# Performance work log

Hardware: AMD Instinct MI355X
Metric: run time of the kernel (lower is better)

Reference implementation:

```python
import jax, jax.numpy as jnp
import numpy as np

EPS = 1e-5


def setup_inputs() -> dict:
    key = jax.random.key(0)
    ks = jax.random.split(key, 12)
    B, S, M, D, H, dh = 8, 512, 512, 1024, 16, 64
    T = S + M
    w_scale = 0.03  # keep attention logits in a sane range (mimics nn.Linear init scale)
    return {
        "x": jax.random.normal(ks[0], (B, S, D), jnp.float32),
        "mem": jax.random.normal(ks[1], (B, M, D), jnp.float32),
        "R": jax.random.normal(ks[2], (T, D), jnp.float32),
        "u": jax.random.normal(ks[3], (1, H, 1, dh), jnp.float32) * 0.1,
        "t": jax.random.normal(ks[4], (1, H, 1, dh), jnp.float32) * 0.1,
        "Wq": jax.random.normal(ks[5], (H * dh, D), jnp.float32) * w_scale,
        "Wk": jax.random.normal(ks[6], (H * dh, D), jnp.float32) * w_scale,
        "Wv": jax.random.normal(ks[7], (H * dh, D), jnp.float32) * w_scale,
        "Wr": jax.random.normal(ks[8], (H * dh, D), jnp.float32) * w_scale,
        "Wo": jax.random.normal(ks[9], (D, H * dh), jnp.float32) * w_scale,
        "gamma": jnp.ones((D,), jnp.float32),
        "beta": jnp.zeros((D,), jnp.float32),
    }


def reference(x, mem, R, u, t, Wq, Wk, Wv, Wr, Wo, gamma, beta):
    B, S, D = x.shape
    H, dh = u.shape[1], u.shape[3]
    h = jnp.concatenate([mem, x], axis=1)          # [B, T, D]
    T = h.shape[1]
    M = T - S

    q = (x @ Wq.T).reshape(B, S, H, dh).transpose(0, 2, 1, 3)   # [B,H,S,dh]
    k = (h @ Wk.T).reshape(B, T, H, dh).transpose(0, 2, 1, 3)   # [B,H,T,dh]
    v = (h @ Wv.T).reshape(B, T, H, dh).transpose(0, 2, 1, 3)   # [B,H,T,dh]
    r = (R[-T:] @ Wr.T).reshape(1, T, H, dh).transpose(0, 2, 1, 3)  # [1,H,T,dh]

    ac = jnp.einsum("bhid,bhjd->bhij", q + u, k)                # [B,H,S,T]
    bd = jnp.einsum("bhid,hjd->bhij", q + t, r[0])              # [B,H,S,T]

    # circulant shift: shifted[..., i, j] = bd[..., i, (j - i + S - 1) % T]
    idx = (jnp.arange(T)[None, :] - jnp.arange(S)[:, None] + S - 1) % T  # [S,T]
    bd = jnp.take_along_axis(bd, idx[None, None], axis=3)

    # causal mask with memory offset: keep j <= i + M (tril(mem_len)), then
    # exact-zero entries (the masked ones) become -inf, matching the original.
    mask = jnp.arange(T)[None, :] <= (jnp.arange(S)[:, None] + M)        # [S,T]
    score = jnp.where(mask[None, None], (ac + bd) / jnp.sqrt(jnp.float32(dh)), 0.0)
    score = jnp.where(score == 0, -jnp.inf, score)
    p = jax.nn.softmax(score, axis=-1)                                   # [B,H,S,T]

    att = jnp.einsum("bhij,bhjd->bhid", p, v).transpose(0, 2, 1, 3).reshape(B, S, H * dh)
    out = att @ Wo.T                                                      # dropout is identity (p=0/eval)

    y = out + x
    mu = jnp.mean(y, axis=-1, keepdims=True)
    var = jnp.var(y, axis=-1, keepdims=True)
    return (y - mu) / jnp.sqrt(var + EPS) * gamma + beta
```

## Files before the change

### kernel.cpp

```cpp
#include <hip/hip_runtime.h>
#include <math.h>

#define BB 8
#define SS 512
#define MM 512
#define TT 1024
#define DD 1024
#define HH 16
#define DH 64

typedef __attribute__((ext_vector_type(8))) short bf16x8;
typedef __attribute__((ext_vector_type(4))) float f32x4;

#define SCL2E 0.1803368801111f
#define DTHR 11.5f

__device__ __forceinline__ ushort f2bf(float f) {
  union { float f; unsigned u; } x; x.f = f;
  unsigned r = x.u + 0x7fffu + ((x.u >> 16) & 1u);
  return (ushort)(r >> 16);
}
__device__ __forceinline__ float bf2f(ushort u) {
  return __builtin_bit_cast(float, ((unsigned)u) << 16);
}

__device__ __forceinline__ void stage16(void* lds, const void* g) {
  __builtin_amdgcn_global_load_lds((const __attribute__((address_space(1))) void*)g,
                                   (__attribute__((address_space(3))) void*)lds, 16, 0, 0);
}

template <int C>
__device__ __forceinline__ float dppf(float x) {
  return __builtin_bit_cast(float,
      __builtin_amdgcn_update_dpp(0, __builtin_bit_cast(int, x), C, 0xF, 0xF, true));
}
__device__ __forceinline__ float redmax16(float x) {
  x = fmaxf(x, dppf<0xB1>(x));
  x = fmaxf(x, dppf<0x4E>(x));
  x = fmaxf(x, dppf<0x141>(x));
  x = fmaxf(x, dppf<0x140>(x));
  return x;
}
__device__ __forceinline__ float redsum16(float x) {
  x += dppf<0xB1>(x);
  x += dppf<0x4E>(x);
  x += dppf<0x141>(x);
  x += dppf<0x140>(x);
  return x;
}
__device__ __forceinline__ float bperm_f(int byteaddr, float v) {
  return __builtin_bit_cast(float,
      __builtin_amdgcn_ds_bpermute(byteaddr, __builtin_bit_cast(int, v)));
}

__global__ __launch_bounds__(256) void cast_all(
    const float* __restrict__ mem, const float* __restrict__ x,
    const float* __restrict__ R, const float* __restrict__ Wq,
    const float* __restrict__ Wk, const float* __restrict__ Wv,
    const float* __restrict__ Wr, const float* __restrict__ Wo,
    ushort* __restrict__ hb, ushort* __restrict__ Rb, ushort* __restrict__ Wqb,
    ushort* __restrict__ Wkb, ushort* __restrict__ Wvb, ushort* __restrict__ Wrb,
    ushort* __restrict__ Wob) {
  const int M1 = 1 << 20;
  int i = (blockIdx.x * 256 + threadIdx.x) * 8;
  const float* src;
  ushort* dst;
  if (i < 4 * M1) {
    src = mem + i;
    dst = hb + (size_t)i + (size_t)(i >> 19) * 524288;
  } else if (i < 8 * M1) {
    int j = i - 4 * M1;
    src = x + j;
    dst = hb + (size_t)j + (size_t)(j >> 19) * 524288 + 524288;
  } else if (i < 9 * M1) {
    src = R + (i - 8 * M1);  dst = Rb + (i - 8 * M1);
  } else if (i < 10 * M1) {
    src = Wq + (i - 9 * M1); dst = Wqb + (i - 9 * M1);
  } else if (i < 11 * M1) {
    src = Wk + (i - 10 * M1); dst = Wkb + (i - 10 * M1);
  } else if (i < 12 * M1) {
    src = Wv + (i - 11 * M1); dst = Wvb + (i - 11 * M1);
  } else if (i < 13 * M1) {
    src = Wr + (i - 12 * M1); dst = Wrb + (i - 12 * M1);
  } else {
    src = Wo + (i - 13 * M1); dst = Wob + (i - 13 * M1);
  }
  float4 a = *(const float4*)(src);
  float4 c = *(const float4*)(src + 4);
  union { bf16x8 v; ushort u[8]; } pk;
  pk.u[0] = f2bf(a.x); pk.u[1] = f2bf(a.y); pk.u[2] = f2bf(a.z); pk.u[3] = f2bf(a.w);
  pk.u[4] = f2bf(c.x); pk.u[5] = f2bf(c.y); pk.u[6] = f2bf(c.z); pk.u[7] = f2bf(c.w);
  *(bf16x8*)(void*)dst = pk.v;
}

__global__ __launch_bounds__(256) void gemm_qkvr(
    const ushort* __restrict__ hb, const ushort* __restrict__ Rbuf,
    const ushort* __restrict__ Wqb, const ushort* __restrict__ Wkb,
    const ushort* __restrict__ Wvb, const ushort* __restrict__ Wrb,
    ushort* __restrict__ qub, ushort* __restrict__ qtb,
    ushort* __restrict__ kbo, ushort* __restrict__ vtb, ushort* __restrict__ rbo,
    const float* __restrict__ uvec, const float* __restrict__ tvec) {
  __shared__ ushort As[128 * 32];
  __shared__ ushort Bs[128 * 32];
  const int bid = (blockIdx.x & 7) * 168 + (blockIdx.x >> 3);
  const ushort* A;
  const ushort* W;
  ushort* C0 = nullptr;
  ushort* C1 = nullptr;
  bool dual = false, qslice = false, vmode = false;
  int mt, nx;
  if (bid < 256) {
    int r = bid; mt = r >> 3; nx = r & 7;
    A = hb; W = Wqb; C0 = qub; C1 = qtb; dual = true; qslice = true;
  } else if (bid < 768) {
    int r = bid - 256; mt = r >> 3; nx = r & 7;
    A = hb; W = Wkb; C0 = kbo;
  } else if (bid < 1280) {
    int r = bid - 768; mt = r >> 3; nx = r & 7;
    A = hb; W = Wvb; C0 = vtb; vmode = true;
  } else {
    int r = bid - 1280; mt = r >> 3; nx = r & 7;
    A = Rbuf; W = Wrb; C0 = rbo;
  }
  const int m0 = mt * 128, n0 = nx * 128;

  const int t = threadIdx.x;
  const int w = t >> 6, l = t & 63;
  const int m16 = l & 15, kg = l >> 4;
  const int wr = w >> 1, wc = w & 1;

  const int c0 = t, c1 = t + 256;
  const ushort* asrc0;
  const ushort* asrc1;
  {
    int gm0 = m0 + (c0 >> 2), gm1 = m0 + (c1 >> 2);
    if (qslice) {
      asrc0 = A + ((size_t)((gm0 >> 9) * TT + MM + (gm0 & 511))) * DD + (c0 & 3) * 8;
      asrc1 = A + ((size_t)((gm1 >> 9) * TT + MM + (gm1 & 511))) * DD + (c1 & 3) * 8;
    } else {
      asrc0 = A + (size_t)gm0 * DD + (c0 & 3) * 8;
      asrc1 = A + (size_t)gm1 * DD + (c1 & 3) * 8;
    }
  }
  const ushort* bsrc0 = W + (size_t)(n0 + (c0 >> 2)) * DD + (c0 & 3) * 8;
  const ushort* bsrc1 = W + (size_t)(n0 + (c1 >> 2)) * DD + (c1 & 3) * 8;
  ushort* adst0 = As + c0 * 8;
  ushort* adst1 = As + c1 * 8;
  ushort* bdst0 = Bs + c0 * 8;
  ushort* bdst1 = Bs + c1 * 8;

  f32x4 acc[4][4];
#pragma unroll
  for (int mi = 0; mi < 4; ++mi)
#pragma unroll
    for (int ni = 0; ni < 4; ++ni) acc[mi][ni] = (f32x4){0.f, 0.f, 0.f, 0.f};

  for (int k0 = 0; k0 < DD; k0 += 32) {
    stage16(adst0, asrc0 + k0);
    stage16(adst1, asrc1 + k0);
    stage16(bdst0, bsrc0 + k0);
    stage16(bdst1, bsrc1 + k0);
    __syncthreads();
    bf16x8 af[4], bfr[4];
#pragma unroll
    for (int mi = 0; mi < 4; ++mi)
      af[mi] = *(const bf16x8*)(const void*)&As[(wr * 64 + mi * 16 + m16) * 32 + kg * 8];
#pragma unroll
    for (int ni = 0; ni < 4; ++ni)
      bfr[ni] = *(const bf16x8*)(const void*)&Bs[(wc * 64 + ni * 16 + m16) * 32 + kg * 8];
#pragma unroll
    for (int mi = 0; mi < 4; ++mi)
#pragma unroll
      for (int ni = 0; ni < 4; ++ni)
        acc[mi][ni] = __builtin_amdgcn_mfma_f32_16x16x32_bf16(af[mi], bfr[ni], acc[mi][ni], 0, 0, 0);
    __syncthreads();
  }

  const int rbase = m0 + wr * 64 + kg * 4;
  const int cbase = n0 + wc * 64 + m16;
  if (vmode) {
    const int bb = m0 >> 10;
    const int tt0 = (m0 & 1023) + wr * 64 + kg * 4;
#pragma unroll
    for (int mi = 0; mi < 4; ++mi)
#pragma unroll
      for (int ni = 0; ni < 4; ++ni) {
        ushort4 o;
        o.x = f2bf(acc[mi][ni][0]); o.y = f2bf(acc[mi][ni][1]);
        o.z = f2bf(acc[mi][ni][2]); o.w = f2bf(acc[mi][ni][3]);
        *(ushort4*)(C0 + ((size_t)(bb * 1024 + cbase + ni * 16) << 10) + tt0 + mi * 16) = o;
      }
  } else if (dual) {
    float uv[4], tv[4];
#pragma unroll
    for (int ni = 0; ni < 4; ++ni) { uv[ni] = uvec[cbase + ni * 16]; tv[ni] = tvec[cbase + ni * 16]; }
#pragma unroll
    for (int mi = 0; mi < 4; ++mi)
#pragma unroll
      for (int ni = 0; ni < 4; ++ni)
#pragma unroll
        for (int rg = 0; rg < 4; ++rg) {
          size_t idx = (size_t)(rbase + mi * 16 + rg) * DD + cbase + ni * 16;
          C0[idx] = f2bf(acc[mi][ni][rg] + uv[ni]);
          C1[idx] = f2bf(acc[mi][ni][rg] + tv[ni]);
        }
  } else {
#pragma unroll
    for (int mi = 0; mi < 4; ++mi)
#pragma unroll
      for (int ni = 0; ni < 4; ++ni)
#pragma unroll
        for (int rg = 0; rg < 4; ++rg)
          C0[(size_t)(rbase + mi * 16 + rg) * DD + cbase + ni * 16] = f2bf(acc[mi][ni][rg]);
  }
}

__global__ __launch_bounds__(256) void gemm_wo(const ushort* __restrict__ A,
                                               const ushort* __restrict__ W,
                                               ushort* __restrict__ Cb) {
  __shared__ ushort As[128 * 32];
  __shared__ ushort Bs[128 * 32];
  const int bid = (blockIdx.x & 7) * 32 + (blockIdx.x >> 3);
  const int mt = bid >> 3, nx = bid & 7;
  const int m0 = mt * 128, n0 = nx * 128;
  const int t = threadIdx.x;
  const int w = t >> 6, l = t & 63;
  const int m16 = l & 15, kg = l >> 4;
  const int wr = w >> 1, wc = w & 1;

  const int c0 = t, c1 = t + 256;
  const ushort* asrc0 = A + (size_t)(m0 + (c0 >> 2)) * DD + (c0 & 3) * 8;
  const ushort* asrc1 = A + (size_t)(m0 + (c1 >> 2)) * DD + (c1 & 3) * 8;
  const ushort* bsrc0 = W + (size_t)(n0 + (c0 >> 2)) * DD + (c0 & 3) * 8;
  const ushort* bsrc1 = W + (size_t)(n0 + (c1 >> 2)) * DD + (c1 & 3) * 8;
  ushort* adst0 = As + c0 * 8;
  ushort* adst1 = As + c1 * 8;
  ushort* bdst0 = Bs + c0 * 8;
  ushort* bdst1 = Bs + c1 * 8;

  f32x4 acc[4][4];
#pragma unroll
  for (int mi = 0; mi < 4; ++mi)
#pragma unroll
    for (int ni = 0; ni < 4; ++ni) acc[mi][ni] = (f32x4){0.f, 0.f, 0.f, 0.f};

  for (int k0 = 0; k0 < DD; k0 += 32) {
    stage16(adst0, asrc0 + k0);
    stage16(adst1, asrc1 + k0);
    stage16(bdst0, bsrc0 + k0);
    stage16(bdst1, bsrc1 + k0);
    __syncthreads();
    bf16x8 af[4], bfr[4];
#pragma unroll
    for (int mi = 0; mi < 4; ++mi)
      af[mi] = *(const bf16x8*)(const void*)&As[(wr * 64 + mi * 16 + m16) * 32 + kg * 8];
#pragma unroll
    for (int ni = 0; ni < 4; ++ni)
      bfr[ni] = *(const bf16x8*)(const void*)&Bs[(wc * 64 + ni * 16 + m16) * 32 + kg * 8];
#pragma unroll
    for (int mi = 0; mi < 4; ++mi)
#pragma unroll
      for (int ni = 0; ni < 4; ++ni)
        acc[mi][ni] = __builtin_amdgcn_mfma_f32_16x16x32_bf16(af[mi], bfr[ni], acc[mi][ni], 0, 0, 0);
    __syncthreads();
  }

  const int rbase = m0 + wr * 64 + kg * 4;
  const int cbase = n0 + wc * 64 + m16;
#pragma unroll
  for (int mi = 0; mi < 4; ++mi)
#pragma unroll
    for (int ni = 0; ni < 4; ++ni)
#pragma unroll
      for (int rg = 0; rg < 4; ++rg)
        Cb[(size_t)(rbase + mi * 16 + rg) * DD + cbase + ni * 16] = f2bf(acc[mi][ni][rg]);
}

__global__ __launch_bounds__(256) void attn_mfma(const ushort* __restrict__ qu,
                                                 const ushort* __restrict__ qt,
                                                 const ushort* __restrict__ kb,
                                                 const ushort* __restrict__ vt,
                                                 const ushort* __restrict__ rb,
                                                 ushort* __restrict__ att) {
  const int w = threadIdx.x >> 6;
  const int l = threadIdx.x & 63;
  const int m16 = l & 15;
  const int kg = l >> 4;
  const int bid = blockIdx.x;
  const int it = 7 - (bid >> 7);
  const int bh = bid & 127;
  const int b = bh >> 4, h = bh & 15;
  const int i0 = it * 64;

  __shared__ ushort Ks[2][4096];
  __shared__ ushort Vs[4096];
  __shared__ ushort Rl[8192];
  __shared__ ushort plds[4][16][72];

  bf16x8 aqu[2], aqt[2];
  {
    const ushort* qrow = qu + ((size_t)(b * SS + i0 + w * 16 + m16)) * DD + h * DH + kg * 8;
    aqu[0] = *(const bf16x8*)(const void*)(qrow);
    aqu[1] = *(const bf16x8*)(const void*)(qrow + 32);
    const ushort* qrow2 = qt + ((size_t)(b * SS + i0 + w * 16 + m16)) * DD + h * DH + kg * 8;
    aqt[0] = *(const bf16x8*)(const void*)(qrow2);
    aqt[1] = *(const bf16x8*)(const void*)(qrow2 + 32);
  }

  int baddr[4];
  bool bsel[4];
#pragma unroll
  for (int rg = 0; rg < 4; ++rg) {
    const int rw = kg * 4 + rg;
    baddr[rg] = (kg * 16 + ((m16 + 15 - rw) & 15)) << 2;
    bsel[rg] = m16 > rw;
  }

  const int c0 = threadIdx.x, c1 = threadIdx.x + 256;
  const int r0 = c0 >> 3, sc0 = ((c0 & 7) * 8) ^ ((r0 & 7) << 3);
  const int r1 = c1 >> 3, sc1 = ((c1 & 7) * 8) ^ ((r1 & 7) << 3);
  const ushort* kp0 = kb + ((size_t)(b * TT) + r0) * DD + h * DH + sc0;
  const ushort* kp1 = kb + ((size_t)(b * TT) + r1) * DD + h * DH + sc1;
  const ushort* vp0 = vt + ((size_t)(b * 1024 + h * DH + r0)) * 1024 + sc0;
  const ushort* vp1 = vt + ((size_t)(b * 1024 + h * DH + r1)) * 1024 + sc1;

  const int cb0 = (kg * 8) ^ ((m16 & 7) << 3);
  const int cb1 = (kg * 8 + 32) ^ ((m16 & 7) << 3);
  int slot64[5];
#pragma unroll
  for (int f = 0; f < 5; ++f)
    slot64[f] = ((496 - i0 - w * 16 + m16 + f * 16) & 127) << 6;

  {
    const int base0 = 448 - i0;
#pragma unroll
    for (int kk = 0; kk < 4; ++kk) {
      int c = threadIdx.x + kk * 256;
      int ro = c >> 3, cc = c & 7;
      int p = base0 + ro;
      int slot = p & 127;
      stage16(Rl + slot * 64 + cc * 8,
              rb + (size_t)p * DD + h * DH + ((cc * 8) ^ ((ro & 7) << 3)));
    }
  }
  stage16(&Ks[0][c0 * 8], kp0);
  stage16(&Ks[0][c1 * 8], kp1);
  stage16(Vs + c0 * 8, vp0);
  stage16(Vs + c1 * 8, vp1);
  kp0 += (size_t)64 * DD; kp1 += (size_t)64 * DD;
  vp0 += 64; vp1 += 64;

  f32x4 O[4];
  float mrow[4], lrow[4];
#pragma unroll
  for (int nt = 0; nt < 4; ++nt) O[nt] = (f32x4){0.f, 0.f, 0.f, 0.f};
#pragma unroll
  for (int rg = 0; rg < 4; ++rg) { mrow[rg] = -1e30f; lrow[rg] = 0.f; }

  const int ntj = it + 9;
  int cur = 0;
  for (int jt = 0; jt < ntj; ++jt) {
    const int j0 = jt * 64;

    if (jt > 0) {
      stage16(Vs + c0 * 8, vp0);
      stage16(Vs + c1 * 8, vp1);
      vp0 += 64; vp1 += 64;
      const int pstart = 512 + j0 - i0;
#pragma unroll
      for (int kk = 0; kk < 2; ++kk) {
        int c = threadIdx.x + kk * 256;
        int ro = c >> 3, cc = c & 7;
        int p = pstart + ro;
        int pc = p < 1023 ? p : 1023;
        int slot = p & 127;
        stage16(Rl + slot * 64 + cc * 8,
                rb + (size_t)pc * DD + h * DH + ((cc * 8) ^ ((ro & 7) << 3)));
      }
    }
    __syncthreads();

    const ushort* kbase = &Ks[cur][0];
    f32x4 ac[4];
#pragma unroll
    for (int nt = 0; nt < 4; ++nt) {
      ac[nt] = (f32x4){0.f, 0.f, 0.f, 0.f};
      const int row = nt * 16 + m16;
#pragma unroll
      for (int ks = 0; ks < 2; ++ks) {
        bf16x8 bk = *(const bf16x8*)(const void*)(kbase + row * 64 + (ks == 0 ? cb0 : cb1));
        ac[nt] = __builtin_amdgcn_mfma_f32_16x16x32_bf16(aqu[ks], bk, ac[nt], 0, 0, 0);
      }
    }

    if (jt + 1 < ntj) {
      stage16(&Ks[cur ^ 1][c0 * 8], kp0);
      stage16(&Ks[cur ^ 1][c1 * 8], kp1);
      kp0 += (size_t)64 * DD; kp1 += (size_t)64 * DD;
    }

    f32x4 bd[5];
#pragma unroll
    for (int f = 0; f < 5; ++f) {
      f32x4 z = (f32x4){0.f, 0.f, 0.f, 0.f};
      bf16x8 b0 = *(const bf16x8*)(const void*)(Rl + slot64[f] + cb0);
      z = __builtin_amdgcn_mfma_f32_16x16x32_bf16(aqt[0], b0, z, 0, 0, 0);
      bf16x8 b1 = *(const bf16x8*)(const void*)(Rl + slot64[f] + cb1);
      bd[f] = __builtin_amdgcn_mfma_f32_16x16x32_bf16(aqt[1], b1, z, 0, 0, 0);
    }
#pragma unroll
    for (int f = 0; f < 5; ++f) slot64[f] = (slot64[f] + 4096) & 8191;

    float sca[4][4];
#pragma unroll
    for (int rg = 0; rg < 4; ++rg) {
      float rr[5];
#pragma unroll
      for (int f = 0; f < 5; ++f) rr[f] = bperm_f(baddr[rg], bd[f][rg]);
#pragma unroll
      for (int nt = 0; nt < 4; ++nt) {
        float bdv = bsel[rg] ? rr[nt + 1] : rr[nt];
        sca[nt][rg] = (ac[nt][rg] + bdv) * SCL2E;
      }
    }
    if (jt == ntj - 1) {
#pragma unroll
      for (int rg = 0; rg < 4; ++rg) {
        const int jmax = i0 + w * 16 + kg * 4 + rg + MM;
#pragma unroll
        for (int nt = 0; nt < 4; ++nt)
          sca[nt][rg] = (j0 + nt * 16 + m16 <= jmax) ? sca[nt][rg] : -1e30f;
      }
    }

    float pmax[4];
#pragma unroll
    for (int rg = 0; rg < 4; ++rg) {
      float pm = fmaxf(fmaxf(sca[0][rg], sca[1][rg]), fmaxf(sca[2][rg], sca[3][rg]));
      pmax[rg] = redmax16(pm);
    }
    bool grow = false;
#pragma unroll
    for (int rg = 0; rg < 4; ++rg) grow = grow || (pmax[rg] > mrow[rg] + DTHR);
    if (__any(grow)) {
#pragma unroll
      for (int rg = 0; rg < 4; ++rg) {
        float mnew = fmaxf(mrow[rg], pmax[rg]);
        float scale = __builtin_amdgcn_exp2f(mrow[rg] - mnew);
        mrow[rg] = mnew;
        lrow[rg] *= scale;
#pragma unroll
        for (int nt = 0; nt < 4; ++nt) O[nt][rg] *= scale;
      }
    }

#pragma unroll
    for (int rg = 0; rg < 4; ++rg) {
      float ps = 0.f;
#pragma unroll
      for (int nt = 0; nt < 4; ++nt) {
        float p = __builtin_amdgcn_exp2f(sca[nt][rg] - mrow[rg]);
        ps += p;
        plds[w][kg * 4 + rg][nt * 16 + m16] = f2bf(p);
      }
      lrow[rg] += redsum16(ps);
    }

#pragma unroll
    for (int ks = 0; ks < 2; ++ks) {
      bf16x8 pa = *(const bf16x8*)(const void*)&plds[w][m16][kg * 8 + ks * 32];
#pragma unroll
      for (int nt = 0; nt < 4; ++nt) {
        bf16x8 vf = *(const bf16x8*)(const void*)(Vs + (nt * 16 + m16) * 64 + (ks == 0 ? cb0 : cb1));
        O[nt] = __builtin_amdgcn_mfma_f32_16x16x32_bf16(pa, vf, O[nt], 0, 0, 0);
      }
    }

    __syncthreads();
    cur ^= 1;
  }

  float linv[4];
#pragma unroll
  for (int rg = 0; rg < 4; ++rg) linv[rg] = 1.f / lrow[rg];
#pragma unroll
  for (int nt = 0; nt < 4; ++nt) {
#pragma unroll
    for (int rg = 0; rg < 4; ++rg) {
      att[((size_t)(b * SS + i0 + w * 16 + kg * 4 + rg)) * DD + h * DH + nt * 16 + m16] =
          f2bf(O[nt][rg] * linv[rg]);
    }
  }
}

__global__ __launch_bounds__(256) void ln_kernel(const ushort* __restrict__ ypre,
                                                 const float* __restrict__ x,
                                                 const float* __restrict__ gamma,
                                                 const float* __restrict__ beta,
                                                 float* __restrict__ out) {
  const int row = blockIdx.x;
  const int t = threadIdx.x;
  const int lane = t & 63, w = t >> 6;
  const ushort* yr = ypre + (size_t)row * DD;
  const float* xr = x + (size_t)row * DD;

  ushort4 yv = *(const ushort4*)(yr + t * 4);
  float4 xv = *(const float4*)(xr + t * 4);
  float v0 = bf2f(yv.x) + xv.x, v1 = bf2f(yv.y) + xv.y;
  float v2 = bf2f(yv.z) + xv.z, v3 = bf2f(yv.w) + xv.w;

  float s = v0 + v1 + v2 + v3;
  float ss = v0 * v0 + v1 * v1 + v2 * v2 + v3 * v3;
  __shared__ float rs[4], rss[4];
#pragma unroll
  for (int off = 32; off; off >>= 1) {
    s += __shfl_xor(s, off);
    ss += __shfl_xor(ss, off);
  }
  if (!lane) { rs[w] = s; rss[w] = ss; }
  __syncthreads();
  s = rs[0] + rs[1] + rs[2] + rs[3];
  ss = rss[0] + rss[1] + rss[2] + rss[3];
  const float mu = s * (1.f / DD);
  const float var = ss * (1.f / DD) - mu * mu;
  const float rstd = rsqrtf(var + 1e-5f);

  float4 g = *(const float4*)(gamma + t * 4);
  float4 be = *(const float4*)(beta + t * 4);
  float4 o;
  o.x = (v0 - mu) * rstd * g.x + be.x;
  o.y = (v1 - mu) * rstd * g.y + be.y;
  o.z = (v2 - mu) * rstd * g.z + be.z;
  o.w = (v3 - mu) * rstd * g.w + be.w;
  *(float4*)(out + (size_t)row * DD + t * 4) = o;
}

extern "C" void kernel_launch(void* const* d_in, const int* in_sizes, int n_in,
                              void* d_out, int out_size, void* d_ws, size_t ws_size,
                              hipStream_t stream) {
  const float* x = (const float*)d_in[0];
  const float* mem = (const float*)d_in[1];
  const float* R = (const float*)d_in[2];
  const float* u = (const float*)d_in[3];
  const float* tv = (const float*)d_in[4];
  const float* Wq = (const float*)d_in[5];
  const float* Wk = (const float*)d_in[6];
  const float* Wv = (const float*)d_in[7];
  const float* Wr = (const float*)d_in[8];
  const float* Wo = (const float*)d_in[9];
  const float* gamma = (const float*)d_in[10];
  const float* beta = (const float*)d_in[11];
  float* out = (float*)d_out;

  ushort* hb = (ushort*)d_ws;
  ushort* Rb = hb + (8u << 20);
  ushort* Wqb = Rb + (1u << 20);
  ushort* Wkb = Wqb + (1u << 20);
  ushort* Wvb = Wkb + (1u << 20);
  ushort* Wrb = Wvb + (1u << 20);
  ushort* Wob = Wrb + (1u << 20);
  ushort* qu_b = Wob + (1u << 20);
  ushort* qt_b = qu_b + (4u << 20);
  ushort* kb = qt_b + (4u << 20);
  ushort* vt = kb + (8u << 20);
  ushort* rb = vt + (8u << 20);
  ushort* att = qu_b;
  ushort* ypre = kb;

  dim3 blk(256);

  cast_all<<<dim3(7168), blk, 0, stream>>>(mem, x, R, Wq, Wk, Wv, Wr, Wo,
                                           hb, Rb, Wqb, Wkb, Wvb, Wrb, Wob);

  gemm_qkvr<<<dim3(1344), blk, 0, stream>>>(hb, Rb, Wqb, Wkb, Wvb, Wrb,
                                            qu_b, qt_b, kb, vt, rb, u, tv);

  attn_mfma<<<dim3(BB * HH * 8), blk, 0, stream>>>(qu_b, qt_b, kb, vt, rb, att);

  gemm_wo<<<dim3(256), blk, 0, stream>>>(att, Wob, ypre);

  ln_kernel<<<dim3(BB * SS), blk, 0, stream>>>(ypre, x, gamma, beta, out);
}
```

Before: 183.9 us.

## Swizzle GEMM LDS tiles to avoid bank conflicts and raise MFMA wave priority

Both projection GEMMs now load global memory into shared memory with an XOR-swizzled column index, and read the fragments back with the matching swizzle. The goal is to remove LDS bank conflicts on the bf16x8 fragment reads. The attention kernel also wraps its MFMA sections in s_setprio(1)/s_setprio(0), so waves issuing matrix ops get scheduling priority over waves doing softmax or loads. The swizzle must map exactly between the store side and the read side, or the GEMM results will be wrong.

```diff
diff --git a/kernel.cpp b/kernel.cpp
--- a/kernel.cpp
+++ b/kernel.cpp
@@ -130,24 +130,27 @@
   const int wr = w >> 1, wc = w & 1;
 
   const int c0 = t, c1 = t + 256;
+  const int scol = (((t & 3) ^ ((t >> 3) & 3)) * 8);
   const ushort* asrc0;
   const ushort* asrc1;
   {
     int gm0 = m0 + (c0 >> 2), gm1 = m0 + (c1 >> 2);
     if (qslice) {
-      asrc0 = A + ((size_t)((gm0 >> 9) * TT + MM + (gm0 & 511))) * DD + (c0 & 3) * 8;
-      asrc1 = A + ((size_t)((gm1 >> 9) * TT + MM + (gm1 & 511))) * DD + (c1 & 3) * 8;
+      asrc0 = A + ((size_t)((gm0 >> 9) * TT + MM + (gm0 & 511))) * DD + scol;
+      asrc1 = A + ((size_t)((gm1 >> 9) * TT + MM + (gm1 & 511))) * DD + scol;
     } else {
-      asrc0 = A + (size_t)gm0 * DD + (c0 & 3) * 8;
-      asrc1 = A + (size_t)gm1 * DD + (c1 & 3) * 8;
-    }
-  }
-  const ushort* bsrc0 = W + (size_t)(n0 + (c0 >> 2)) * DD + (c0 & 3) * 8;
-  const ushort* bsrc1 = W + (size_t)(n0 + (c1 >> 2)) * DD + (c1 & 3) * 8;
+      asrc0 = A + (size_t)gm0 * DD + scol;
+      asrc1 = A + (size_t)gm1 * DD + scol;
+    }
+  }
+  const ushort* bsrc0 = W + (size_t)(n0 + (c0 >> 2)) * DD + scol;
+  const ushort* bsrc1 = W + (size_t)(n0 + (c1 >> 2)) * DD + scol;
   ushort* adst0 = As + c0 * 8;
   ushort* adst1 = As + c1 * 8;
   ushort* bdst0 = Bs + c0 * 8;
   ushort* bdst1 = Bs + c1 * 8;
+
+  const int cbx = ((kg ^ ((m16 >> 1) & 3)) << 3);
 
   f32x4 acc[4][4];
 #pragma unroll
@@ -164,10 +167,10 @@
     bf16x8 af[4], bfr[4];
 #pragma unroll
     for (int mi = 0; mi < 4; ++mi)
-      af[mi] = *(const bf16x8*)(const void*)&As[(wr * 64 + mi * 16 + m16) * 32 + kg * 8];
+      af[mi] = *(const bf16x8*)(const void*)&As[(wr * 64 + mi * 16 + m16) * 32 + cbx];
 #pragma unroll
     for (int ni = 0; ni < 4; ++ni)
-      bfr[ni] = *(const bf16x8*)(const void*)&Bs[(wc * 64 + ni * 16 + m16) * 32 + kg * 8];
+      bfr[ni] = *(const bf16x8*)(const void*)&Bs[(wc * 64 + ni * 16 + m16) * 32 + cbx];
 #pragma unroll
     for (int mi = 0; mi < 4; ++mi)
 #pragma unroll
@@ -229,14 +232,17 @@
   const int wr = w >> 1, wc = w & 1;
 
   const int c0 = t, c1 = t + 256;
-  const ushort* asrc0 = A + (size_t)(m0 + (c0 >> 2)) * DD + (c0 & 3) * 8;
-  const ushort* asrc1 = A + (size_t)(m0 + (c1 >> 2)) * DD + (c1 & 3) * 8;
-  const ushort* bsrc0 = W + (size_t)(n0 + (c0 >> 2)) * DD + (c0 & 3) * 8;
-  const ushort* bsrc1 = W + (size_t)(n0 + (c1 >> 2)) * DD + (c1 & 3) * 8;
+  const int scol = (((t & 3) ^ ((t >> 3) & 3)) * 8);
+  const ushort* asrc0 = A + (size_t)(m0 + (c0 >> 2)) * DD + scol;
+  const ushort* asrc1 = A + (size_t)(m0 + (c1 >> 2)) * DD + scol;
+  const ushort* bsrc0 = W + (size_t)(n0 + (c0 >> 2)) * DD + scol;
+  const ushort* bsrc1 = W + (size_t)(n0 + (c1 >> 2)) * DD + scol;
   ushort* adst0 = As + c0 * 8;
   ushort* adst1 = As + c1 * 8;
   ushort* bdst0 = Bs + c0 * 8;
   ushort* bdst1 = Bs + c1 * 8;
+
+  const int cbx = ((kg ^ ((m16 >> 1) & 3)) << 3);
 
   f32x4 acc[4][4];
 #pragma unroll
@@ -253,10 +259,10 @@
     bf16x8 af[4], bfr[4];
 #pragma unroll
     for (int mi = 0; mi < 4; ++mi)
-      af[mi] = *(const bf16x8*)(const void*)&As[(wr * 64 + mi * 16 + m16) * 32 + kg * 8];
+      af[mi] = *(const bf16x8*)(const void*)&As[(wr * 64 + mi * 16 + m16) * 32 + cbx];
 #pragma unroll
     for (int ni = 0; ni < 4; ++ni)
-      bfr[ni] = *(const bf16x8*)(const void*)&Bs[(wc * 64 + ni * 16 + m16) * 32 + kg * 8];
+      bfr[ni] = *(const bf16x8*)(const void*)&Bs[(wc * 64 + ni * 16 + m16) * 32 + cbx];
 #pragma unroll
     for (int mi = 0; mi < 4; ++mi)
 #pragma unroll
@@ -382,6 +388,7 @@
 
     const ushort* kbase = &Ks[cur][0];
     f32x4 ac[4];
+    __builtin_amdgcn_s_setprio(1);
 #pragma unroll
     for (int nt = 0; nt < 4; ++nt) {
       ac[nt] = (f32x4){0.f, 0.f, 0.f, 0.f};
@@ -392,6 +399,7 @@
         ac[nt] = __builtin_amdgcn_mfma_f32_16x16x32_bf16(aqu[ks], bk, ac[nt], 0, 0, 0);
       }
     }
+    __builtin_amdgcn_s_setprio(0);
 
     if (jt + 1 < ntj) {
       stage16(&Ks[cur ^ 1][c0 * 8], kp0);
@@ -400,6 +408,7 @@
     }
 
     f32x4 bd[5];
+    __builtin_amdgcn_s_setprio(1);
 #pragma unroll
     for (int f = 0; f < 5; ++f) {
       f32x4 z = (f32x4){0.f, 0.f, 0.f, 0.f};
@@ -408,6 +417,7 @@
       bf16x8 b1 = *(const bf16x8*)(const void*)(Rl + slot64[f] + cb1);
       bd[f] = __builtin_amdgcn_mfma_f32_16x16x32_bf16(aqt[1], b1, z, 0, 0, 0);
     }
+    __builtin_amdgcn_s_setprio(0);
 #pragma unroll
     for (int f = 0; f < 5; ++f) slot64[f] = (slot64[f] + 4096) & 8191;
 
@@ -466,6 +476,7 @@
       lrow[rg] += redsum16(ps);
     }
 
+    __builtin_amdgcn_s_setprio(1);
 #pragma unroll
     for (int ks = 0; ks < 2; ++ks) {
       bf16x8 pa = *(const bf16x8*)(const void*)&plds[w][m16][kg * 8 + ks * 32];
@@ -475,6 +486,7 @@
         O[nt] = __builtin_amdgcn_mfma_f32_16x16x32_bf16(pa, vf, O[nt], 0, 0, 0);
       }
     }
+    __builtin_amdgcn_s_setprio(0);
 
     __syncthreads();
     cur ^= 1;
```

After: 178.6 us. 2.9% less time.
